# Kernel tuning notes

Measured on AMD Instinct MI355X. Metric: run time of the kernel, lower is better.

Reference implementation:

```python
import jax, jax.numpy as jnp
import numpy as np

B = 8192
D = 626
TEMP = 0.25
EPS = 1e-8


def setup_inputs() -> dict:
    key = jax.random.key(0)
    k1, k2 = jax.random.split(key)
    anchors = jax.random.normal(k1, (B, D), dtype=jnp.float32)
    poss = jax.random.normal(k2, (B, D), dtype=jnp.float32)
    return {"anchors": anchors, "poss": poss}


def reference(anchors, poss):
    # Full pairwise cosine similarity: S[i, j] = cos(anchors[i], poss[j]).
    # torch.nn.CosineSimilarity: dot(x, y) / max(||x|| * ||y||, eps)
    na = jnp.linalg.norm(anchors, axis=1)          # [B]
    np_ = jnp.linalg.norm(poss, axis=1)            # [B]
    dots = anchors @ poss.T                        # [B, B]
    S = dots / jnp.maximum(na[:, None] * np_[None, :], EPS)

    diag = jnp.diagonal(S)                         # [B] positive-pair cosines
    logits = S / TEMP
    # loss_i = -log( exp(logits_ii) / sum_j exp(logits_ij) )
    loss = jax.nn.logsumexp(logits, axis=1) - jnp.diagonal(logits)

    n = S.shape[0]
    cos_an_pos = diag.mean()
    cos_an_neg = ((S.sum(axis=1) - diag) / (n - 1)).mean()
    return (loss.mean(), cos_an_pos, cos_an_neg)
```

## Files before the change

kernel.cpp:

```cpp
#include <hip/hip_runtime.h>
#include <stdint.h>

#define B_N   8192
#define D_K   626
#define KPAD  640
#define BK    128
#define KSTEPS 5
#define BM    128
#define BN    128
#define COL_CHUNKS 16
#define TILES_PER_CHUNK 4
#define FIN_BLOCKS 16

typedef __attribute__((ext_vector_type(4))) float f32x4;
typedef __attribute__((ext_vector_type(4))) int   i32x4;
typedef __attribute__((ext_vector_type(8))) int   i32x8;
typedef __attribute__((ext_vector_type(16))) float f32x16;

__device__ __forceinline__ void async16(const unsigned char* g, unsigned char* l) {
    __builtin_amdgcn_global_load_lds(
        (const __attribute__((address_space(1))) unsigned int*)(const void*)g,
        (__attribute__((address_space(3))) unsigned int*)(void*)l,
        16, 0, 0);
}

__global__ __launch_bounds__(256) void normalize_kernel(
    const float* __restrict__ A, const float* __restrict__ P,
    unsigned char* __restrict__ Af8, unsigned char* __restrict__ Pf8,
    float* __restrict__ rowexp, float* __restrict__ rowsum, float* __restrict__ acc)
{
    const int which = blockIdx.y;
    const float* srcM = which ? P : A;
    unsigned char* dstM = which ? Pf8 : Af8;
    const int t  = threadIdx.x;
    const int wv = t >> 6;
    const int L  = t & 63;
    const int rowBase = blockIdx.x * 8 + wv * 2;

    if (which == 0) {
        const int rb = blockIdx.x * 8;
        if (t < 8) { rowexp[rb + t] = 0.0f; rowsum[rb + t] = 0.0f; }
        if (blockIdx.x == 0 && t < 4) acc[t] = 0.0f;
    }

    #pragma unroll
    for (int j = 0; j < 2; ++j) {
        const int r = rowBase + j;
        const float2* s2 = (const float2*)(srcM + (size_t)r * D_K);

        float2 a0 = s2[2 * L];       float2 a1 = s2[2 * L + 1];
        float2 b0 = s2[2 * L + 128]; float2 b1 = s2[2 * L + 129];
        float2 c0 = {0.f, 0.f},      c1 = {0.f, 0.f};
        if (L < 28)       { c0 = s2[2 * L + 256]; c1 = s2[2 * L + 257]; }
        else if (L == 28) { c0 = s2[312]; }

        float ss = a0.x * a0.x + a0.y * a0.y + a1.x * a1.x + a1.y * a1.y
                 + b0.x * b0.x + b0.y * b0.y + b1.x * b1.x + b1.y * b1.y
                 + c0.x * c0.x + c0.y * c0.y + c1.x * c1.x + c1.y * c1.y;
        #pragma unroll
        for (int off = 32; off; off >>= 1) ss += __shfl_xor(ss, off, 64);
        const float rn = rsqrtf(ss);

        int* d4 = (int*)(dstM + (size_t)r * KPAD);
        int pk0 = __builtin_amdgcn_cvt_pk_fp8_f32(a0.x * rn, a0.y * rn, 0, false);
        pk0 = __builtin_amdgcn_cvt_pk_fp8_f32(a1.x * rn, a1.y * rn, pk0, true);
        d4[L] = pk0;
        int pk1 = __builtin_amdgcn_cvt_pk_fp8_f32(b0.x * rn, b0.y * rn, 0, false);
        pk1 = __builtin_amdgcn_cvt_pk_fp8_f32(b1.x * rn, b1.y * rn, pk1, true);
        d4[L + 64] = pk1;
        if (L < 32) {
            int pk2 = __builtin_amdgcn_cvt_pk_fp8_f32(c0.x * rn, c0.y * rn, 0, false);
            pk2 = __builtin_amdgcn_cvt_pk_fp8_f32(c1.x * rn, c1.y * rn, pk2, true);
            d4[L + 128] = pk2;
        }
    }
}

__global__ __launch_bounds__(256, 2) void gemm_fused_kernel(
    const unsigned char* __restrict__ Af8, const unsigned char* __restrict__ Pf8,
    float* __restrict__ rowexp, float* __restrict__ rowsum, float* __restrict__ diag)
{
    __shared__ __align__(16) unsigned char sA[2][BM * BK];
    __shared__ __align__(16) unsigned char sB[2][BN * BK];

    const int t    = threadIdx.x;
    const int lane = t & 63;
    const int w    = t >> 6;
    const int wr   = w >> 1;
    const int wc   = w & 1;
    const int rA   = lane & 31;
    const int h    = lane >> 5;
    const int rx   = (rA & 7) ^ ((rA >> 4) & 1);

    const int rowBase = blockIdx.x * BM;
    const int chunk   = blockIdx.y;

    const int p0 = t, p1 = t + 256, p2 = t + 512, p3 = t + 768;
    const int r0 = p0 >> 3, r1 = p1 >> 3, r2 = p2 >> 3, r3 = p3 >> 3;
    const size_t g0 = (size_t)r0 * KPAD
                    + (size_t)((((p0 & 7) ^ (r0 & 7) ^ ((r0 >> 4) & 1))) * 16);
    const size_t g1 = (size_t)r1 * KPAD
                    + (size_t)((((p1 & 7) ^ (r1 & 7) ^ ((r1 >> 4) & 1))) * 16);
    const size_t g2 = (size_t)r2 * KPAD
                    + (size_t)((((p2 & 7) ^ (r2 & 7) ^ ((r2 >> 4) & 1))) * 16);
    const size_t g3 = (size_t)r3 * KPAD
                    + (size_t)((((p3 & 7) ^ (r3 & 7) ^ ((r3 >> 4) & 1))) * 16);

    const unsigned char* Ab = Af8 + (size_t)rowBase * KPAD;
    const unsigned char* PbChunk = Pf8 + (size_t)(chunk * TILES_PER_CHUNK) * BN * KPAD;

    float psum[2][16], pexp[2][16];
    #pragma unroll
    for (int i = 0; i < 2; ++i)
        #pragma unroll
        for (int j = 0; j < 16; ++j) { psum[i][j] = 0.0f; pexp[i][j] = 0.0f; }

    const f32x16 z16 = {0.f,0.f,0.f,0.f,0.f,0.f,0.f,0.f,
                        0.f,0.f,0.f,0.f,0.f,0.f,0.f,0.f};
    f32x16 acc[2][2];
    acc[0][0] = z16; acc[0][1] = z16; acc[1][0] = z16; acc[1][1] = z16;

    {
        async16(Ab + g0, &sA[0][p0 * 16]);
        async16(Ab + g1, &sA[0][p1 * 16]);
        async16(Ab + g2, &sA[0][p2 * 16]);
        async16(Ab + g3, &sA[0][p3 * 16]);
        async16(PbChunk + g0, &sB[0][p0 * 16]);
        async16(PbChunk + g1, &sB[0][p1 * 16]);
        async16(PbChunk + g2, &sB[0][p2 * 16]);
        async16(PbChunk + g3, &sB[0][p3 * 16]);
    }

    int par = 0;
    for (int ct = 0; ct < TILES_PER_CHUNK; ++ct) {
        #pragma unroll 1
        for (int ks = 0; ks < KSTEPS; ++ks) {
            __syncthreads();

            int nks = ks + 1, nct = ct;
            if (nks == KSTEPS) { nks = 0; ++nct; }
            if (nct < TILES_PER_CHUNK) {
                const int nxt = par ^ 1;
                const size_t nkOff = (size_t)nks * BK;
                const unsigned char* PbN = PbChunk + (size_t)nct * BN * KPAD + nkOff;
                const unsigned char* AbN = Ab + nkOff;
                async16(AbN + g0, &sA[nxt][p0 * 16]);
                async16(AbN + g1, &sA[nxt][p1 * 16]);
                async16(AbN + g2, &sA[nxt][p2 * 16]);
                async16(AbN + g3, &sA[nxt][p3 * 16]);
                async16(PbN + g0, &sB[nxt][p0 * 16]);
                async16(PbN + g1, &sB[nxt][p1 * 16]);
                async16(PbN + g2, &sB[nxt][p2 * 16]);
                async16(PbN + g3, &sB[nxt][p3 * 16]);
            }

            #pragma unroll
            for (int kb = 0; kb < 2; ++kb) {
                const int c0 = kb * 4 + 2 * h;
                const int s0 = ((c0    ) ^ rx) * 16;
                const int s1 = ((c0 ^ 1) ^ rx) * 16;

                i32x8 aF[2], bF[2];
                #pragma unroll
                for (int mi = 0; mi < 2; ++mi) {
                    const unsigned char* base = &sA[par][(wr * 64 + mi * 32 + rA) * BK];
                    i32x4 lo = *(const i32x4*)(base + s0);
                    i32x4 hi = *(const i32x4*)(base + s1);
                    aF[mi] = __builtin_shufflevector(lo, hi, 0, 1, 2, 3, 4, 5, 6, 7);
                }
                #pragma unroll
                for (int ni = 0; ni < 2; ++ni) {
                    const unsigned char* base = &sB[par][(wc * 64 + ni * 32 + rA) * BK];
                    i32x4 lo = *(const i32x4*)(base + s0);
                    i32x4 hi = *(const i32x4*)(base + s1);
                    bF[ni] = __builtin_shufflevector(lo, hi, 0, 1, 2, 3, 4, 5, 6, 7);
                }

                #pragma unroll
                for (int mi = 0; mi < 2; ++mi)
                    #pragma unroll
                    for (int ni = 0; ni < 2; ++ni)
                        acc[mi][ni] = __builtin_amdgcn_mfma_scale_f32_32x32x64_f8f6f4(
                            aF[mi], bF[ni], acc[mi][ni],
                            0 , 0 ,
                            0, 0x7F , 0, 0x7F );
            }
            par ^= 1;
        }

        const int colBase = (chunk * TILES_PER_CHUNK + ct) * BN;

        if (rowBase == colBase && wr == wc) {
            #pragma unroll
            for (int mi = 0; mi < 2; ++mi)
                #pragma unroll
                for (int rg = 0; rg < 16; ++rg) {
                    const int row32 = (rg & 3) + 8 * (rg >> 2) + 4 * h;
                    if (rA == row32)
                        diag[rowBase + wr * 64 + mi * 32 + row32] = acc[mi][mi][rg];
                }
        }

        #pragma unroll
        for (int mi = 0; mi < 2; ++mi) {
            #pragma unroll
            for (int rg = 0; rg < 16; ++rg) {
                const float S0 = acc[mi][0][rg];
                const float S1 = acc[mi][1][rg];
                psum[mi][rg] += S0 + S1;
                pexp[mi][rg] += __expf(S0 * 4.0f) + __expf(S1 * 4.0f);
            }
        }
        acc[0][0] = z16; acc[0][1] = z16; acc[1][0] = z16; acc[1][1] = z16;
    }

    #pragma unroll
    for (int off = 1; off <= 16; off <<= 1) {
        #pragma unroll
        for (int mi = 0; mi < 2; ++mi)
            #pragma unroll
            for (int rg = 0; rg < 16; ++rg) {
                psum[mi][rg] += __shfl_xor(psum[mi][rg], off, 64);
                pexp[mi][rg] += __shfl_xor(pexp[mi][rg], off, 64);
            }
    }
    if (rA == 0) {
        #pragma unroll
        for (int mi = 0; mi < 2; ++mi)
            #pragma unroll
            for (int rg = 0; rg < 16; ++rg) {
                const int gr = rowBase + wr * 64 + mi * 32
                             + (rg & 3) + 8 * (rg >> 2) + 4 * h;
                atomicAdd(&rowsum[gr], psum[mi][rg]);
                atomicAdd(&rowexp[gr], pexp[mi][rg]);
            }
    }
}

__global__ __launch_bounds__(256) void finalize_kernel(
    const float* __restrict__ rowexp, const float* __restrict__ rowsum,
    const float* __restrict__ diag, float* __restrict__ acc, float* __restrict__ out)
{
    const int t = threadIdx.x;
    float ls = 0.f, ds = 0.f, ns = 0.f;
    for (int i = blockIdx.x * 256 + t; i < B_N; i += FIN_BLOCKS * 256) {
        const float d = diag[i];
        ls += __logf(rowexp[i]) - d * 4.0f;
        ds += d;
        ns += (rowsum[i] - d);
    }
    #pragma unroll
    for (int off = 32; off; off >>= 1) {
        ls += __shfl_down(ls, off, 64);
        ds += __shfl_down(ds, off, 64);
        ns += __shfl_down(ns, off, 64);
    }
    __shared__ float sl[4], sd[4], sn[4];
    if ((t & 63) == 0) { sl[t >> 6] = ls; sd[t >> 6] = ds; sn[t >> 6] = ns; }
    __syncthreads();
    if (t == 0) {
        atomicAdd(acc + 0, sl[0] + sl[1] + sl[2] + sl[3]);
        atomicAdd(acc + 1, sd[0] + sd[1] + sd[2] + sd[3]);
        atomicAdd(acc + 2, sn[0] + sn[1] + sn[2] + sn[3]);
        __threadfence();
        const int done = (int)atomicAdd((unsigned int*)(acc + 3), 1u);
        if (done == FIN_BLOCKS - 1) {
            const float L  = atomicAdd(acc + 0, 0.0f);
            const float Dm = atomicAdd(acc + 1, 0.0f);
            const float Nn = atomicAdd(acc + 2, 0.0f);
            out[0] = L / (float)B_N;
            out[1] = Dm / (float)B_N;
            out[2] = (Nn / (float)(B_N - 1)) / (float)B_N;
        }
    }
}

__global__ __launch_bounds__(256) void fb_norm(
    const float* __restrict__ A, const float* __restrict__ P,
    float* __restrict__ rna, float* __restrict__ rnp, float* __restrict__ acc)
{
    const int r = blockIdx.x;
    const float* src = blockIdx.y ? P : A;
    const int t = threadIdx.x;
    float ss = 0.f;
    for (int k = t; k < D_K; k += 256) { float v = src[(size_t)r * D_K + k]; ss += v * v; }
    #pragma unroll
    for (int off = 32; off; off >>= 1) ss += __shfl_down(ss, off, 64);
    __shared__ float sred[4];
    if ((t & 63) == 0) sred[t >> 6] = ss;
    __syncthreads();
    if (t == 0) {
        const float rn = rsqrtf(sred[0] + sred[1] + sred[2] + sred[3]);
        (blockIdx.y ? rnp : rna)[r] = rn;
    }
    if (blockIdx.x == 0 && blockIdx.y == 0 && t < 3) acc[t] = 0.0f;
}

__global__ __launch_bounds__(256) void fb_main(
    const float* __restrict__ A, const float* __restrict__ P,
    const float* __restrict__ rna, const float* __restrict__ rnp,
    float* __restrict__ acc)
{
    __shared__ float sa[D_K];
    __shared__ float red[12];
    const int i = blockIdx.x;
    const int t = threadIdx.x;
    const float rn = rna[i];
    for (int k = t; k < D_K; k += 256) sa[k] = A[(size_t)i * D_K + k] * rn;
    __syncthreads();
    const int w = t >> 6, lane = t & 63;
    float we = 0.f, wsum = 0.f, wd = 0.f;
    for (int j = w; j < B_N; j += 4) {
        float dot = 0.f;
        const float* p = P + (size_t)j * D_K;
        for (int k = lane; k < D_K; k += 64) dot += sa[k] * p[k];
        #pragma unroll
        for (int off = 32; off; off >>= 1) dot += __shfl_xor(dot, off, 64);
        const float S = dot * rnp[j];
        we += __expf(S * 4.0f);
        wsum += S;
        if (j == i) wd = S;
    }
    if (lane == 0) { red[w] = we; red[4 + w] = wsum; red[8 + w] = wd; }
    __syncthreads();
    if (t == 0) {
        const float E  = red[0] + red[1] + red[2] + red[3];
        const float Sm = red[4] + red[5] + red[6] + red[7];
        const float Dd = red[8] + red[9] + red[10] + red[11];
        atomicAdd(acc + 0, __logf(E) - 4.0f * Dd);
        atomicAdd(acc + 1, Dd);
        atomicAdd(acc + 2, Sm - Dd);
    }
}

__global__ void fb_fin(const float* __restrict__ acc, float* __restrict__ out)
{
    out[0] = acc[0] / (float)B_N;
    out[1] = acc[1] / (float)B_N;
    out[2] = acc[2] / ((float)(B_N - 1) * (float)B_N);
}

extern "C" void kernel_launch(void* const* d_in, const int* in_sizes, int n_in,
                              void* d_out, int out_size, void* d_ws, size_t ws_size,
                              hipStream_t stream)
{
    const float* A = (const float*)d_in[0];
    const float* P = (const float*)d_in[1];
    float* out = (float*)d_out;
    char* ws = (char*)d_ws;

    const size_t AF8_OFF  = 0;
    const size_t PF8_OFF  = AF8_OFF + (size_t)B_N * KPAD;
    const size_t REXP_OFF = PF8_OFF + (size_t)B_N * KPAD;
    const size_t RSUM_OFF = REXP_OFF + (size_t)B_N * sizeof(float);
    const size_t DIAG_OFF = RSUM_OFF + (size_t)B_N * sizeof(float);
    const size_t ACC_OFF  = DIAG_OFF + (size_t)B_N * sizeof(float);
    const size_t MAIN_REQ = ACC_OFF + 16;

    if (ws_size >= MAIN_REQ) {
        unsigned char* Af8 = (unsigned char*)(ws + AF8_OFF);
        unsigned char* Pf8 = (unsigned char*)(ws + PF8_OFF);
        float* rowexp = (float*)(ws + REXP_OFF);
        float* rowsum = (float*)(ws + RSUM_OFF);
        float* diag   = (float*)(ws + DIAG_OFF);
        float* acc    = (float*)(ws + ACC_OFF);

        normalize_kernel<<<dim3(B_N / 8, 2), 256, 0, stream>>>(A, P, Af8, Pf8,
                                                               rowexp, rowsum, acc);
        gemm_fused_kernel<<<dim3(B_N / BM, COL_CHUNKS), 256, 0, stream>>>(
            Af8, Pf8, rowexp, rowsum, diag);
        finalize_kernel<<<FIN_BLOCKS, 256, 0, stream>>>(rowexp, rowsum, diag, acc, out);
    } else {
        float* rna = (float*)ws;
        float* rnp = rna + B_N;
        float* acc = rnp + B_N;
        fb_norm<<<dim3(B_N, 2), 256, 0, stream>>>(A, P, rna, rnp, acc);
        fb_main<<<B_N, 256, 0, stream>>>(A, P, rna, rnp, acc);
        fb_fin<<<1, 1, 0, stream>>>(acc, out);
    }
}
```

Measured before the change: 150.5 us.

## Load B operand fragments directly from global memory into registers, bypassing LDS

Drops the shared-memory staging buffer for the P (B) operand. Each wave now loads its B fragments straight from global memory into registers at the start of every k-step, while A stays double-buffered in LDS through async loads. This halves LDS traffic and LDS footprint, which may allow more occupancy. The cost is exposed global-load latency, because the B loads are issued right before they are used with no prefetch, and the two waves that share a column tile each fetch the same B rows.

New measurement: 194.0 us. 28.9% more time.

```diff
diff --git a/kernel.cpp b/kernel.cpp
--- a/kernel.cpp
+++ b/kernel.cpp
@@ -12,7 +12,6 @@
 #define TILES_PER_CHUNK 4
 #define FIN_BLOCKS 16
 
-typedef __attribute__((ext_vector_type(4))) float f32x4;
 typedef __attribute__((ext_vector_type(4))) int   i32x4;
 typedef __attribute__((ext_vector_type(8))) int   i32x8;
 typedef __attribute__((ext_vector_type(16))) float f32x16;
@@ -81,7 +80,6 @@
     float* __restrict__ rowexp, float* __restrict__ rowsum, float* __restrict__ diag)
 {
     __shared__ __align__(16) unsigned char sA[2][BM * BK];
-    __shared__ __align__(16) unsigned char sB[2][BN * BK];
 
     const int t    = threadIdx.x;
     const int lane = t & 63;
@@ -109,6 +107,9 @@
     const unsigned char* Ab = Af8 + (size_t)rowBase * KPAD;
     const unsigned char* PbChunk = Pf8 + (size_t)(chunk * TILES_PER_CHUNK) * BN * KPAD;
 
+    const size_t bOff0 = (size_t)(wc * 64 + 0 * 32 + rA) * KPAD + (size_t)(h * 32);
+    const size_t bOff1 = (size_t)(wc * 64 + 1 * 32 + rA) * KPAD + (size_t)(h * 32);
+
     float psum[2][16], pexp[2][16];
     #pragma unroll
     for (int i = 0; i < 2; ++i)
@@ -120,38 +121,40 @@
     f32x16 acc[2][2];
     acc[0][0] = z16; acc[0][1] = z16; acc[1][0] = z16; acc[1][1] = z16;
 
-    {
-        async16(Ab + g0, &sA[0][p0 * 16]);
-        async16(Ab + g1, &sA[0][p1 * 16]);
-        async16(Ab + g2, &sA[0][p2 * 16]);
-        async16(Ab + g3, &sA[0][p3 * 16]);
-        async16(PbChunk + g0, &sB[0][p0 * 16]);
-        async16(PbChunk + g1, &sB[0][p1 * 16]);
-        async16(PbChunk + g2, &sB[0][p2 * 16]);
-        async16(PbChunk + g3, &sB[0][p3 * 16]);
-    }
+    async16(Ab + g0, &sA[0][p0 * 16]);
+    async16(Ab + g1, &sA[0][p1 * 16]);
+    async16(Ab + g2, &sA[0][p2 * 16]);
+    async16(Ab + g3, &sA[0][p3 * 16]);
 
     int par = 0;
     for (int ct = 0; ct < TILES_PER_CHUNK; ++ct) {
+        const unsigned char* PbTile = PbChunk + (size_t)ct * BN * KPAD;
+
         #pragma unroll 1
         for (int ks = 0; ks < KSTEPS; ++ks) {
             __syncthreads();
+
+            const unsigned char* pB = PbTile + (size_t)ks * BK;
+            i32x4 bLo[2][2], bHi[2][2];
+            #pragma unroll
+            for (int kb = 0; kb < 2; ++kb) {
+                const unsigned char* pK = pB + kb * 64;
+                bLo[kb][0] = *(const i32x4*)(pK + bOff0);
+                bHi[kb][0] = *(const i32x4*)(pK + bOff0 + 16);
+                bLo[kb][1] = *(const i32x4*)(pK + bOff1);
+                bHi[kb][1] = *(const i32x4*)(pK + bOff1 + 16);
+            }
+            __builtin_amdgcn_sched_barrier(0);
 
             int nks = ks + 1, nct = ct;
             if (nks == KSTEPS) { nks = 0; ++nct; }
             if (nct < TILES_PER_CHUNK) {
                 const int nxt = par ^ 1;
-                const size_t nkOff = (size_t)nks * BK;
-                const unsigned char* PbN = PbChunk + (size_t)nct * BN * KPAD + nkOff;
-                const unsigned char* AbN = Ab + nkOff;
+                const unsigned char* AbN = Ab + (size_t)nks * BK;
                 async16(AbN + g0, &sA[nxt][p0 * 16]);
                 async16(AbN + g1, &sA[nxt][p1 * 16]);
                 async16(AbN + g2, &sA[nxt][p2 * 16]);
                 async16(AbN + g3, &sA[nxt][p3 * 16]);
-                async16(PbN + g0, &sB[nxt][p0 * 16]);
-                async16(PbN + g1, &sB[nxt][p1 * 16]);
-                async16(PbN + g2, &sB[nxt][p2 * 16]);
-                async16(PbN + g3, &sB[nxt][p3 * 16]);
             }
 
             #pragma unroll
@@ -168,13 +171,10 @@
                     i32x4 hi = *(const i32x4*)(base + s1);
                     aF[mi] = __builtin_shufflevector(lo, hi, 0, 1, 2, 3, 4, 5, 6, 7);
                 }
-                #pragma unroll
-                for (int ni = 0; ni < 2; ++ni) {
-                    const unsigned char* base = &sB[par][(wc * 64 + ni * 32 + rA) * BK];
-                    i32x4 lo = *(const i32x4*)(base + s0);
-                    i32x4 hi = *(const i32x4*)(base + s1);
-                    bF[ni] = __builtin_shufflevector(lo, hi, 0, 1, 2, 3, 4, 5, 6, 7);
-                }
+                bF[0] = __builtin_shufflevector(bLo[kb][0], bHi[kb][0],
+                                                0, 1, 2, 3, 4, 5, 6, 7);
+                bF[1] = __builtin_shufflevector(bLo[kb][1], bHi[kb][1],
+                                                0, 1, 2, 3, 4, 5, 6, 7);
 
                 #pragma unroll
                 for (int mi = 0; mi < 2; ++mi)
```
